# Kernel tuning notes

Hardware: AMD Instinct MI355X
Metric: run time of the kernel (lower is better)

## Reference

```python
import jax, jax.numpy as jnp
import numpy as np

B, L, J, D_MODEL, N_HIDDEN = 8, 2048, 2048, 1024, 1024


def setup_inputs() -> dict:
    key = jax.random.key(0)
    ks = jax.random.split(key, 6)
    scale = 1.0 / np.sqrt(D_MODEL)
    return {
        "q": jax.random.normal(ks[0], (B, L, D_MODEL), dtype=jnp.float32),
        "k": jax.random.normal(ks[1], (B, J, D_MODEL), dtype=jnp.float32),
        "v": jax.random.normal(ks[2], (B, J, D_MODEL), dtype=jnp.float32),
        "mask": jnp.zeros((B, L, J), dtype=jnp.float32),
        # Linear(d_model, n_hidden, bias=False) weights, stored [n_hidden, d_model] like torch
        "W_q": jax.random.normal(ks[3], (N_HIDDEN, D_MODEL), dtype=jnp.float32) * scale,
        "W_k": jax.random.normal(ks[4], (N_HIDDEN, D_MODEL), dtype=jnp.float32) * scale,
        "W_v": jax.random.normal(ks[5], (N_HIDDEN, D_MODEL), dtype=jnp.float32) * scale,
    }


def reference(q, k, v, mask, W_q, W_k, W_v):
    # Linear projections (torch Linear: x @ W.T)
    qp = jnp.einsum('bld,hd->blh', q, W_q)
    kp = jnp.einsum('bjd,hd->bjh', k, W_k)
    vp = jnp.einsum('bjd,hd->bjh', v, W_v)
    # scaled dot-product scores [B, L, J]
    scores = jnp.einsum('blh,bjh->blj', qp, kp) / jnp.sqrt(jnp.float32(N_HIDDEN)).astype(qp.dtype)
    scores = scores + mask
    attn = jax.nn.softmax(scores, axis=-1)
    return jnp.einsum('blj,bjh->blh', attn, vp)
```

## Files before the change

kernel.cpp:

```cpp
#include <hip/hip_runtime.h>
#include <hip/hip_fp16.h>

typedef _Float16 f16;
typedef __attribute__((ext_vector_type(8))) _Float16 f16x8;
typedef __attribute__((ext_vector_type(4))) _Float16 f16x4;
typedef __attribute__((ext_vector_type(4))) float f32x4;

#define BM 256
#define BN 256
#define BK 64

__device__ __forceinline__ void gll16(const void* src, void* dst) {
  __builtin_amdgcn_global_load_lds((const __attribute__((address_space(1))) void*)src,
                                   (__attribute__((address_space(3))) void*)dst,
                                   16, 0, 0);
}

template<int MODE>
__global__ __launch_bounds__(512, 2)
void gemm_bt(const f16* __restrict__ Aall, const f16* __restrict__ Ball,
             void* __restrict__ Call,
             int M, int N, int K, int lda, int ldb, int ldc,
             long strideA, long strideB, long strideC,
             const float* __restrict__ maskAll, long strideMask,
             float* __restrict__ lvec, float scale)
{
  __shared__ __align__(16) f16 smA[2][BM * BK];
  __shared__ __align__(16) f16 smB[2][BN * BK];

  const int z = blockIdx.z;
  const f16* A = Aall + (long)z * strideA;
  const f16* B = Ball + (long)z * strideB;

  const int tid  = threadIdx.x;
  const int wid  = tid >> 6;
  const int lane = tid & 63;
  const int wm = wid >> 2;
  const int wn = wid & 3;
  const int lr = lane & 15;
  const int g  = lane >> 4;

  const long brow = (long)blockIdx.y * BM;
  const long bcol = (long)blockIdx.x * BN;
  const int  nt   = K / BK;

  f32x4 acc[8][4] = {};

  auto stA = [&](int buf, int t, int i0) {
    #pragma unroll
    for (int ii = 0; ii < 2; ++ii) {
      int c   = (i0 + ii) * 512 + tid;
      int row = c >> 3;
      int sl  = (c & 7) ^ (row & 7);
      gll16(A + (brow + row) * (long)lda + t * BK + sl * 8, &smA[buf][c * 8]);
    }
  };
  auto stB = [&](int buf, int t, int i0) {
    #pragma unroll
    for (int ii = 0; ii < 2; ++ii) {
      int c   = (i0 + ii) * 512 + tid;
      int row = c >> 3;
      int sl  = (c & 7) ^ (row & 7);
      gll16(B + (bcol + row) * (long)ldb + t * BK + sl * 8, &smB[buf][c * 8]);
    }
  };
  auto ld = [&](const f16* base, int r, int ks) -> f16x8 {
    return *(const f16x8*)(base + r * BK + (((ks << 2) + g) ^ (r & 7)) * 8);
  };

  stA(0, 0, 0); stA(0, 0, 2); stB(0, 0, 0); stB(0, 0, 2);
  asm volatile("s_waitcnt vmcnt(0)" ::: "memory");
  __builtin_amdgcn_s_barrier();

  for (int kt = 0; kt < nt; ++kt) {
    const int cur = kt & 1;
    const f16* sa = smA[cur];
    const f16* sb = smB[cur];
    const bool pf = (kt + 1 < nt);
    f16x8 af[4], bf[4];

    #pragma unroll
    for (int n = 0; n < 4; ++n) bf[n] = ld(sb, wn * 64 + n * 16 + lr, 0);
    #pragma unroll
    for (int m = 0; m < 4; ++m) af[m] = ld(sa, wm * 128 + m * 16 + lr, 0);
    if (pf) { stA(cur ^ 1, kt + 1, 0); stA(cur ^ 1, kt + 1, 2); }
    __builtin_amdgcn_s_barrier();
    asm volatile("s_waitcnt lgkmcnt(0)" ::: "memory");
    __builtin_amdgcn_sched_barrier(0);
    __builtin_amdgcn_s_setprio(1);
    #pragma unroll
    for (int m = 0; m < 4; ++m)
      #pragma unroll
      for (int n = 0; n < 4; ++n)
        acc[m][n] = __builtin_amdgcn_mfma_f32_16x16x32_f16(af[m], bf[n], acc[m][n], 0, 0, 0);
    __builtin_amdgcn_s_setprio(0);
    __builtin_amdgcn_s_barrier();

    #pragma unroll
    for (int m = 0; m < 4; ++m) af[m] = ld(sa, wm * 128 + 64 + m * 16 + lr, 0);
    if (pf) { stB(cur ^ 1, kt + 1, 0); stB(cur ^ 1, kt + 1, 2); }
    __builtin_amdgcn_s_barrier();
    asm volatile("s_waitcnt lgkmcnt(0)" ::: "memory");
    __builtin_amdgcn_sched_barrier(0);
    __builtin_amdgcn_s_setprio(1);
    #pragma unroll
    for (int m = 0; m < 4; ++m)
      #pragma unroll
      for (int n = 0; n < 4; ++n)
        acc[m + 4][n] = __builtin_amdgcn_mfma_f32_16x16x32_f16(af[m], bf[n], acc[m + 4][n], 0, 0, 0);
    __builtin_amdgcn_s_setprio(0);
    __builtin_amdgcn_s_barrier();

    #pragma unroll
    for (int n = 0; n < 4; ++n) bf[n] = ld(sb, wn * 64 + n * 16 + lr, 1);
    #pragma unroll
    for (int m = 0; m < 4; ++m) af[m] = ld(sa, wm * 128 + m * 16 + lr, 1);
    __builtin_amdgcn_s_barrier();
    asm volatile("s_waitcnt lgkmcnt(0)" ::: "memory");
    __builtin_amdgcn_sched_barrier(0);
    __builtin_amdgcn_s_setprio(1);
    #pragma unroll
    for (int m = 0; m < 4; ++m)
      #pragma unroll
      for (int n = 0; n < 4; ++n)
        acc[m][n] = __builtin_amdgcn_mfma_f32_16x16x32_f16(af[m], bf[n], acc[m][n], 0, 0, 0);
    __builtin_amdgcn_s_setprio(0);
    __builtin_amdgcn_s_barrier();

    #pragma unroll
    for (int m = 0; m < 4; ++m) af[m] = ld(sa, wm * 128 + 64 + m * 16 + lr, 1);
    __builtin_amdgcn_s_barrier();
    asm volatile("s_waitcnt lgkmcnt(0)" ::: "memory");
    __builtin_amdgcn_sched_barrier(0);
    __builtin_amdgcn_s_setprio(1);
    #pragma unroll
    for (int m = 0; m < 4; ++m)
      #pragma unroll
      for (int n = 0; n < 4; ++n)
        acc[m + 4][n] = __builtin_amdgcn_mfma_f32_16x16x32_f16(af[m], bf[n], acc[m + 4][n], 0, 0, 0);
    __builtin_amdgcn_s_setprio(0);
    __builtin_amdgcn_sched_barrier(0);
    asm volatile("s_waitcnt vmcnt(0)" ::: "memory");
    __builtin_amdgcn_s_barrier();
  }

  const int rb = (lane >> 4) * 4;

  if (MODE == 0) {
    f16* C = (f16*)Call + (long)z * strideC;
    #pragma unroll
    for (int m = 0; m < 8; ++m)
      #pragma unroll
      for (int j = 0; j < 4; ++j) {
        long grow = brow + wm * 128 + m * 16 + rb + j;
        #pragma unroll
        for (int n = 0; n < 4; ++n) {
          long gcol = bcol + wn * 64 + n * 16 + lr;
          C[grow * ldc + gcol] = (f16)acc[m][n][j];
        }
      }
  } else if (MODE == 1) {
    f16* C = (f16*)Call + (long)z * strideC;
    const float* mask = maskAll + (long)z * strideMask;
    #pragma unroll
    for (int m = 0; m < 8; ++m)
      #pragma unroll
      for (int j = 0; j < 4; ++j) {
        long grow = brow + wm * 128 + m * 16 + rb + j;
        float s = 0.f;
        #pragma unroll
        for (int n = 0; n < 4; ++n) {
          long gcol = bcol + wn * 64 + n * 16 + lr;
          float p = __expf(acc[m][n][j] * scale + mask[grow * ldc + gcol]);
          C[grow * ldc + gcol] = (f16)p;
          s += p;
        }
        s += __shfl_xor(s, 1);
        s += __shfl_xor(s, 2);
        s += __shfl_xor(s, 4);
        s += __shfl_xor(s, 8);
        if (lr == 0)
          lvec[((long)z * M + grow) * 32 + blockIdx.x * 4 + wn] = s;
      }
  } else {
    float* C = (float*)Call + (long)z * strideC;
    #pragma unroll
    for (int m = 0; m < 8; ++m)
      #pragma unroll
      for (int j = 0; j < 4; ++j) {
        long grow = brow + wm * 128 + m * 16 + rb + j;
        float inv = 1.0f / lvec[(long)z * M + grow];
        #pragma unroll
        for (int n = 0; n < 4; ++n) {
          long gcol = bcol + wn * 64 + n * 16 + lr;
          C[grow * ldc + gcol] = acc[m][n][j] * inv;
        }
      }
  }
}

__global__ void cvt_all(const float* __restrict__ q, const float* __restrict__ k,
                        const float* __restrict__ v, const float* __restrict__ Wq,
                        const float* __restrict__ Wk, const float* __restrict__ Wv,
                        f16* __restrict__ qf, f16* __restrict__ kf, f16* __restrict__ vf,
                        f16* __restrict__ Wqf, f16* __restrict__ Wkf, f16* __restrict__ Wvf)
{
  const long NQ4 = 4194304, NW4 = 262144;
  const long total = 3 * NQ4 + 3 * NW4;
  for (long i = (long)blockIdx.x * blockDim.x + threadIdx.x; i < total;
       i += (long)gridDim.x * blockDim.x) {
    const float* src; f16* dst; long j = i;
    if      (j <     NQ4)           { src = q;  dst = qf; }
    else if (j < 2 * NQ4)           { src = k;  dst = kf;  j -= NQ4; }
    else if (j < 3 * NQ4)           { src = v;  dst = vf;  j -= 2 * NQ4; }
    else if (j < 3 * NQ4 + NW4)     { src = Wq; dst = Wqf; j -= 3 * NQ4; }
    else if (j < 3 * NQ4 + 2 * NW4) { src = Wk; dst = Wkf; j -= 3 * NQ4 + NW4; }
    else                            { src = Wv; dst = Wvf; j -= 3 * NQ4 + 2 * NW4; }
    float4 vv = ((const float4*)src)[j];
    f16x4 o;
    o[0] = (f16)vv.x; o[1] = (f16)vv.y; o[2] = (f16)vv.z; o[3] = (f16)vv.w;
    ((f16x4*)dst)[j] = o;
  }
}

__global__ void reduce_l(const float* __restrict__ lpart, float* __restrict__ lsum, int n) {
  int i = blockIdx.x * blockDim.x + threadIdx.x;
  if (i < n) {
    float s = 0.f;
    #pragma unroll
    for (int j = 0; j < 32; ++j) s += lpart[(long)i * 32 + j];
    lsum[i] = s;
  }
}

extern "C" void kernel_launch(void* const* d_in, const int* in_sizes, int n_in,
                              void* d_out, int out_size, void* d_ws, size_t ws_size,
                              hipStream_t stream)
{
  const float* q    = (const float*)d_in[0];
  const float* k    = (const float*)d_in[1];
  const float* v    = (const float*)d_in[2];
  const float* mask = (const float*)d_in[3];
  const float* Wq   = (const float*)d_in[4];
  const float* Wk   = (const float*)d_in[5];
  const float* Wv   = (const float*)d_in[6];
  float* out = (float*)d_out;
  char*  ws  = (char*)d_ws;

  f16* qf  = (f16*)(ws + 0);
  f16* kf  = (f16*)(ws + 33554432);
  f16* vf  = (f16*)(ws + 67108864);
  f16* Pm  = (f16*)(ws + 0);
  f16* Wqf = (f16*)(ws + 100663296);
  f16* Wkf = (f16*)(ws + 102760448);
  f16* Wvf = (f16*)(ws + 104857600);
  f16* qp  = (f16*)(ws + 106954752);
  f16* kp  = (f16*)(ws + 140509184);
  f16* vpT = (f16*)(ws + 174063616);
  float* lpart = (float*)(ws + 207618048);
  float* lsum  = (float*)(ws + 209715200);

  const long L = 2048, J = 2048, D = 1024, H = 1024;

  cvt_all<<<dim3(2048), dim3(256), 0, stream>>>(q, k, v, Wq, Wk, Wv, qf, kf, vf, Wqf, Wkf, Wvf);

  gemm_bt<0><<<dim3(1024 / BN, 16384 / BM, 1), dim3(512), 0, stream>>>(
      qf, Wqf, qp, 16384, 1024, 1024, 1024, 1024, 1024,
      0, 0, 0, nullptr, 0, nullptr, 0.f);
  gemm_bt<0><<<dim3(1024 / BN, 16384 / BM, 1), dim3(512), 0, stream>>>(
      kf, Wkf, kp, 16384, 1024, 1024, 1024, 1024, 1024,
      0, 0, 0, nullptr, 0, nullptr, 0.f);
  gemm_bt<0><<<dim3(2048 / BN, 1024 / BM, 8), dim3(512), 0, stream>>>(
      Wvf, vf, vpT, 1024, 2048, 1024, 1024, 1024, 2048,
      0, J * D, H * J, nullptr, 0, nullptr, 0.f);

  gemm_bt<1><<<dim3(2048 / BN, 2048 / BM, 8), dim3(512), 0, stream>>>(
      qp, kp, Pm, 2048, 2048, 1024, 1024, 1024, 2048,
      L * H, J * H, L * J, mask, L * J, lpart, 0.03125f);

  reduce_l<<<dim3(16384 / 256), dim3(256), 0, stream>>>(lpart, lsum, 16384);

  gemm_bt<2><<<dim3(1024 / BN, 2048 / BM, 8), dim3(512), 0, stream>>>(
      Pm, vpT, out, 2048, 1024, 2048, 2048, 2048, 1024,
      L * J, H * J, L * H, nullptr, 0, lsum, 0.f);
}
```

Baseline: 380.6 us.

## Triple-buffer LDS with BK=32, prefetch two tiles ahead, swizzle workgroup order

Halves the K tile to 32 and moves from double to triple buffering in shared memory, so global loads for tile kt+2 are issued while tile kt is computed. The barrier waits only on the older loads via vmcnt(4). It also drops the XOR swizzle on LDS, which may bring back bank conflicts on the 64-byte row stride. Finally it remaps the linear workgroup id so that blocks are spread round-robin across 8 groups, likely for XCD/L2 locality. The costs are twice as many loop iterations and barriers per unit of K, and the possible LDS bank conflicts.

```diff
diff --git a/kernel.cpp b/kernel.cpp
--- a/kernel.cpp
+++ b/kernel.cpp
@@ -8,7 +8,7 @@
 
 #define BM 256
 #define BN 256
-#define BK 64
+#define BK 32
 
 __device__ __forceinline__ void gll16(const void* src, void* dst) {
   __builtin_amdgcn_global_load_lds((const __attribute__((address_space(1))) void*)src,
@@ -25,10 +25,17 @@
              const float* __restrict__ maskAll, long strideMask,
              float* __restrict__ lvec, float scale)
 {
-  __shared__ __align__(16) f16 smA[2][BM * BK];
-  __shared__ __align__(16) f16 smB[2][BN * BK];
-
-  const int z = blockIdx.z;
+  __shared__ __align__(16) f16 smA[3][BM * BK];
+  __shared__ __align__(16) f16 smB[3][BN * BK];
+
+  unsigned gx = gridDim.x, gy = gridDim.y;
+  unsigned id = (blockIdx.z * gy + blockIdx.y) * gx + blockIdx.x;
+  unsigned nwg = gx * gy * gridDim.z;
+  unsigned swz = (id & 7) * (nwg >> 3) + (id >> 3);
+  unsigned bx = swz % gx, rem = swz / gx;
+  unsigned by = rem % gy, bz = rem / gy;
+
+  const int z = bz;
   const f16* A = Aall + (long)z * strideA;
   const f16* B = Ball + (long)z * strideB;
 
@@ -40,50 +47,49 @@
   const int lr = lane & 15;
   const int g  = lane >> 4;
 
-  const long brow = (long)blockIdx.y * BM;
-  const long bcol = (long)blockIdx.x * BN;
+  const long brow = (long)by * BM;
+  const long bcol = (long)bx * BN;
   const int  nt   = K / BK;
 
   f32x4 acc[8][4] = {};
 
-  auto stA = [&](int buf, int t, int i0) {
-    #pragma unroll
-    for (int ii = 0; ii < 2; ++ii) {
-      int c   = (i0 + ii) * 512 + tid;
-      int row = c >> 3;
-      int sl  = (c & 7) ^ (row & 7);
-      gll16(A + (brow + row) * (long)lda + t * BK + sl * 8, &smA[buf][c * 8]);
+  auto stA = [&](int buf, int t) {
+    #pragma unroll
+    for (int i = 0; i < 2; ++i) {
+      int c   = i * 512 + tid;
+      int row = c >> 2;
+      gll16(A + (brow + row) * (long)lda + t * BK + (c & 3) * 8, &smA[buf][c * 8]);
     }
   };
-  auto stB = [&](int buf, int t, int i0) {
-    #pragma unroll
-    for (int ii = 0; ii < 2; ++ii) {
-      int c   = (i0 + ii) * 512 + tid;
-      int row = c >> 3;
-      int sl  = (c & 7) ^ (row & 7);
-      gll16(B + (bcol + row) * (long)ldb + t * BK + sl * 8, &smB[buf][c * 8]);
+  auto stB = [&](int buf, int t) {
+    #pragma unroll
+    for (int i = 0; i < 2; ++i) {
+      int c   = i * 512 + tid;
+      int row = c >> 2;
+      gll16(B + (bcol + row) * (long)ldb + t * BK + (c & 3) * 8, &smB[buf][c * 8]);
     }
   };
-  auto ld = [&](const f16* base, int r, int ks) -> f16x8 {
-    return *(const f16x8*)(base + r * BK + (((ks << 2) + g) ^ (r & 7)) * 8);
+  auto ld = [&](const f16* base, int r) -> f16x8 {
+    return *(const f16x8*)(base + r * BK + g * 8);
   };
 
-  stA(0, 0, 0); stA(0, 0, 2); stB(0, 0, 0); stB(0, 0, 2);
-  asm volatile("s_waitcnt vmcnt(0)" ::: "memory");
+  stA(0, 0); stB(0, 0);
+  stA(1, 1); stB(1, 1);
+  asm volatile("s_waitcnt vmcnt(4)" ::: "memory");
   __builtin_amdgcn_s_barrier();
 
+  int b0 = 0, bn = 2;
   for (int kt = 0; kt < nt; ++kt) {
-    const int cur = kt & 1;
-    const f16* sa = smA[cur];
-    const f16* sb = smB[cur];
-    const bool pf = (kt + 1 < nt);
+    const f16* sa = smA[b0];
+    const f16* sb = smB[b0];
+    const bool pf = (kt + 2 < nt);
     f16x8 af[4], bf[4];
 
     #pragma unroll
-    for (int n = 0; n < 4; ++n) bf[n] = ld(sb, wn * 64 + n * 16 + lr, 0);
-    #pragma unroll
-    for (int m = 0; m < 4; ++m) af[m] = ld(sa, wm * 128 + m * 16 + lr, 0);
-    if (pf) { stA(cur ^ 1, kt + 1, 0); stA(cur ^ 1, kt + 1, 2); }
+    for (int n = 0; n < 4; ++n) bf[n] = ld(sb, wn * 64 + n * 16 + lr);
+    #pragma unroll
+    for (int m = 0; m < 4; ++m) af[m] = ld(sa, wm * 128 + m * 16 + lr);
+    if (pf) stA(bn, kt + 2);
     __builtin_amdgcn_s_barrier();
     asm volatile("s_waitcnt lgkmcnt(0)" ::: "memory");
     __builtin_amdgcn_sched_barrier(0);
@@ -97,38 +103,8 @@
     __builtin_amdgcn_s_barrier();
 
     #pragma unroll
-    for (int m = 0; m < 4; ++m) af[m] = ld(sa, wm * 128 + 64 + m * 16 + lr, 0);
-    if (pf) { stB(cur ^ 1, kt + 1, 0); stB(cur ^ 1, kt + 1, 2); }
-    __builtin_amdgcn_s_barrier();
-    asm volatile("s_waitcnt lgkmcnt(0)" ::: "memory");
-    __builtin_amdgcn_sched_barrier(0);
-    __builtin_amdgcn_s_setprio(1);
-    #pragma unroll
-    for (int m = 0; m < 4; ++m)
-      #pragma unroll
-      for (int n = 0; n < 4; ++n)
-        acc[m + 4][n] = __builtin_amdgcn_mfma_f32_16x16x32_f16(af[m], bf[n], acc[m + 4][n], 0, 0, 0);
-    __builtin_amdgcn_s_setprio(0);
-    __builtin_amdgcn_s_barrier();
-
-    #pragma unroll
-    for (int n = 0; n < 4; ++n) bf[n] = ld(sb, wn * 64 + n * 16 + lr, 1);
-    #pragma unroll
-    for (int m = 0; m < 4; ++m) af[m] = ld(sa, wm * 128 + m * 16 + lr, 1);
-    __builtin_amdgcn_s_barrier();
-    asm volatile("s_waitcnt lgkmcnt(0)" ::: "memory");
-    __builtin_amdgcn_sched_barrier(0);
-    __builtin_amdgcn_s_setprio(1);
-    #pragma unroll
-    for (int m = 0; m < 4; ++m)
-      #pragma unroll
-      for (int n = 0; n < 4; ++n)
-        acc[m][n] = __builtin_amdgcn_mfma_f32_16x16x32_f16(af[m], bf[n], acc[m][n], 0, 0, 0);
-    __builtin_amdgcn_s_setprio(0);
-    __builtin_amdgcn_s_barrier();
-
-    #pragma unroll
-    for (int m = 0; m < 4; ++m) af[m] = ld(sa, wm * 128 + 64 + m * 16 + lr, 1);
+    for (int m = 0; m < 4; ++m) af[m] = ld(sa, wm * 128 + 64 + m * 16 + lr);
+    if (pf) stB(bn, kt + 2);
     __builtin_amdgcn_s_barrier();
     asm volatile("s_waitcnt lgkmcnt(0)" ::: "memory");
     __builtin_amdgcn_sched_barrier(0);
@@ -140,8 +116,11 @@
         acc[m + 4][n] = __builtin_amdgcn_mfma_f32_16x16x32_f16(af[m], bf[n], acc[m + 4][n], 0, 0, 0);
     __builtin_amdgcn_s_setprio(0);
     __builtin_amdgcn_sched_barrier(0);
-    asm volatile("s_waitcnt vmcnt(0)" ::: "memory");
-    __builtin_amdgcn_s_barrier();
+    if (pf) { asm volatile("s_waitcnt vmcnt(4)" ::: "memory"); }
+    else    { asm volatile("s_waitcnt vmcnt(0)" ::: "memory"); }
+    __builtin_amdgcn_s_barrier();
+    b0 = b0 + 1 == 3 ? 0 : b0 + 1;
+    bn = bn + 1 == 3 ? 0 : bn + 1;
   }
 
   const int rb = (lane >> 4) * 4;
@@ -180,7 +159,7 @@
         s += __shfl_xor(s, 4);
         s += __shfl_xor(s, 8);
         if (lr == 0)
-          lvec[((long)z * M + grow) * 32 + blockIdx.x * 4 + wn] = s;
+          lvec[((long)z * M + grow) * 32 + bx * 4 + wn] = s;
       }
   } else {
     float* C = (float*)Call + (long)z * strideC;
```

After: 385.3 us. About the same (+1.2%).
